# Performance work log

Hardware: AMD Instinct MI355X
Metric: run time of the kernel (lower is better)

Reference implementation:

```python
import jax, jax.numpy as jnp
import numpy as np

N_NODES = 100000
N_EDGES = 1600000
D = 128
EPS = 0.0  # train_eps=False -> constant


def setup_inputs() -> dict:
    key = jax.random.key(0)
    k = jax.random.split(key, 6)
    s = 1.0 / np.sqrt(D)
    return {
        "X": jax.random.normal(k[0], (N_NODES, D), dtype=jnp.float32),
        "W1": jax.random.normal(k[1], (D, D), dtype=jnp.float32) * s,
        "b1": jnp.zeros((D,), dtype=jnp.float32),
        "W2": jax.random.normal(k[2], (D, D), dtype=jnp.float32) * s,
        "b2": jnp.zeros((D,), dtype=jnp.float32),
        "edge_src": jax.random.randint(k[3], (N_EDGES,), 0, N_NODES, dtype=jnp.int32),
        "edge_dst": jax.random.randint(k[4], (N_EDGES,), 0, N_NODES, dtype=jnp.int32),
    }


def reference(X, W1, b1, W2, b2, edge_src, edge_dst):
    # v2v sum aggregation: agg[i] = sum_{j in N(i)} X[j]
    msgs = X[edge_src]  # (E, D) gather
    agg = jax.ops.segment_sum(msgs, edge_dst, num_segments=N_NODES)  # (N, D)
    h = (1.0 + EPS) * X + agg
    # MLP: Linear -> ReLU -> Linear
    h = jax.nn.relu(h @ W1 + b1)
    out = h @ W2 + b2
    return out
```

## Files before the change

### kernel.cpp

```cpp
#include <hip/hip_runtime.h>
#include <hip/hip_bf16.h>

#define N_NODES 100000
#define N_EDGES 1600000
#define D 128

#define NBINS 196
#define BINSHIFT 9
#define EPB 8192
#define RBLK 196
#define EBUF_CAP 8960

#define MID_SORT_BLOCKS 196
#define MID_W_BLOCKS 8
#define MID_CVT_BLOCKS 3125

#define PADK 136

typedef __bf16 bf16x8 __attribute__((ext_vector_type(8)));
typedef short short8 __attribute__((ext_vector_type(8)));
typedef float f32x4 __attribute__((ext_vector_type(4)));

__device__ __forceinline__ unsigned short f2bf(float f) {
  union { float f; unsigned u; } c; c.f = f;
  unsigned u = c.u;
  u += 0x7FFFu + ((u >> 16) & 1u);
  return (unsigned short)(u >> 16);
}
__device__ __forceinline__ float bflo(unsigned u) {
  union { unsigned u; float f; } c; c.u = u << 16; return c.f;
}
__device__ __forceinline__ float bfhi(unsigned u) {
  union { unsigned u; float f; } c; c.u = u & 0xFFFF0000u; return c.f;
}

__launch_bounds__(512)
__global__ void k_bin2(const int* __restrict__ esrc, const int* __restrict__ edst,
                       unsigned* __restrict__ binbuf, int* __restrict__ cntmatT,
                       int* __restrict__ startmatT) {
  __shared__ unsigned lbuf[EPB];
  __shared__ int cnt[NBINS];
  __shared__ int base[NBINS];
  __shared__ int cur[NBINS];
  __shared__ int scanb[256];
  const int b = blockIdx.x, t = threadIdx.x;
  const int e0 = b * EPB;
  const int ne = min(EPB, N_EDGES - e0);

  for (int i = t; i < NBINS; i += 512) { cnt[i] = 0; cur[i] = 0; }
  __syncthreads();
  for (int i = t; i < ne; i += 512)
    atomicAdd(&cnt[edst[e0 + i] >> BINSHIFT], 1);
  __syncthreads();
  if (t < 256) scanb[t] = (t < NBINS) ? cnt[t] : 0;
  __syncthreads();
  for (int d = 1; d < 256; d <<= 1) {
    int x = 0;
    if (t < 256 && t >= d) x = scanb[t - d];
    __syncthreads();
    if (t < 256) scanb[t] += x;
    __syncthreads();
  }
  if (t < NBINS) base[t] = scanb[t] - cnt[t];
  __syncthreads();
  for (int i = t; i < ne; i += 512) {
    int d = edst[e0 + i];
    int s = esrc[e0 + i];
    int bi = d >> BINSHIFT;
    int pos = base[bi] + atomicAdd(&cur[bi], 1);
    lbuf[pos] = ((unsigned)(d & 511) << 17) | (unsigned)s;
  }
  __syncthreads();
  uint4* dst4 = (uint4*)(binbuf + (size_t)b * EPB);
  const uint4* src4 = (const uint4*)lbuf;
  for (int i = t; i < EPB / 4; i += 512) dst4[i] = src4[i];
  if (t < NBINS) {
    cntmatT[t * RBLK + b] = cnt[t];
    startmatT[t * RBLK + b] = base[t];
  }
}

__launch_bounds__(512)
__global__ void k_mid(const unsigned* __restrict__ binbuf, const int* __restrict__ cntmatT,
                      const int* __restrict__ startmatT,
                      int* __restrict__ srt, int* __restrict__ deg, int* __restrict__ offs,
                      const float* __restrict__ X, unsigned short* __restrict__ Xb,
                      const float* __restrict__ W1, const float* __restrict__ W2,
                      unsigned short* __restrict__ Wimg) {
  const int b = blockIdx.x, t = threadIdx.x;

  if (b < MID_SORT_BLOCKS) {
    __shared__ unsigned ebuf[EBUF_CAP];
    __shared__ int hist[512];
    __shared__ int scn[512];
    __shared__ int rcnt[RBLK];
    __shared__ int roff[RBLK];
    __shared__ int eoff[RBLK];
    __shared__ int colsc[256];

    for (int r = t; r < RBLK; r += 512) {
      rcnt[r] = cntmatT[b * RBLK + r];
      roff[r] = startmatT[b * RBLK + r];
    }
    int cs = 0;
    if (t < NBINS) {
      const uint4* row = (const uint4*)(cntmatT + t * RBLK);
#pragma unroll 7
      for (int j = 0; j < RBLK / 4; ++j) {
        uint4 v = row[j];
        cs += (int)(v.x + v.y + v.z + v.w);
      }
    }
    if (t < 256) colsc[t] = (t < NBINS) ? cs : 0;
    __syncthreads();
    for (int d = 1; d < 256; d <<= 1) {
      int x = 0;
      if (t < 256 && t >= d) x = colsc[t - d];
      __syncthreads();
      if (t < 256) colsc[t] += x;
      __syncthreads();
    }
    const int total = cntmatT ? 0 : 0;
    (void)total;
    const int mytotal_holder = 0; (void)mytotal_holder;
    __syncthreads();
    const int mytotal = colsc[b] - ((b == 0) ? 0 : colsc[b - 1]);
    const int gbase = (b == 0) ? 0 : colsc[b - 1];

    if (t < 256) scn[t] = (t < RBLK) ? rcnt[t] : 0;
    __syncthreads();
    for (int d = 1; d < 256; d <<= 1) {
      int x = 0;
      if (t < 256 && t >= d) x = scn[t - d];
      __syncthreads();
      if (t < 256) scn[t] += x;
      __syncthreads();
    }
    if (t < RBLK) eoff[t] = scn[t] - rcnt[t];
    __syncthreads();

    const int wv = t >> 6, ln = t & 63;
    for (int r = wv; r < RBLK; r += 8) {
      const unsigned* src = binbuf + (size_t)r * EPB + roff[r];
      int c = rcnt[r], o = eoff[r];
      for (int i = ln; i < c; i += 64) ebuf[o + i] = src[i];
    }
    hist[t] = 0;
    __syncthreads();

    for (int i = t; i < mytotal; i += 512)
      atomicAdd(&hist[ebuf[i] >> 17], 1);
    __syncthreads();
    int v = hist[t];
    scn[t] = v;
    __syncthreads();
    for (int d = 1; d < 512; d <<= 1) {
      int x = (t >= d) ? scn[t - d] : 0;
      __syncthreads();
      scn[t] += x;
      __syncthreads();
    }
    int n = (b << BINSHIFT) + t;
    if (n < N_NODES) {
      deg[n] = v;
      offs[n] = gbase + scn[t] - v;
    }
    hist[t] = scn[t] - v;
    __syncthreads();
    for (int i = t; i < mytotal; i += 512) {
      unsigned e = ebuf[i];
      int pos = atomicAdd(&hist[e >> 17], 1);
      srt[gbase + pos] = (int)(e & 0x1FFFFu);
    }
    return;
  }
  if (b < MID_SORT_BLOCKS + MID_W_BLOCKS) {
    int bb = b - MID_SORT_BLOCKS;
    const float* W = (bb & 4) ? W2 : W1;
    unsigned short* img = Wimg + ((bb & 4) ? 128 * PADK : 0);
    int k0 = (bb & 3) * 32;
#pragma unroll
    for (int it = 0; it < 8; ++it) {
      int idx = it * 512 + t;
      int k = k0 + (idx >> 7), n = idx & 127;
      img[n * PADK + k] = f2bf(W[k * 128 + n]);
    }
    return;
  }
  size_t i = ((size_t)(b - MID_SORT_BLOCKS - MID_W_BLOCKS) * 512 + t) * 8;
  const float4* p = (const float4*)(X + i);
  float4 a = p[0], c = p[1];
  short8 s;
  s[0] = f2bf(a.x); s[1] = f2bf(a.y); s[2] = f2bf(a.z); s[3] = f2bf(a.w);
  s[4] = f2bf(c.x); s[5] = f2bf(c.y); s[6] = f2bf(c.z); s[7] = f2bf(c.w);
  *(short8*)(Xb + i) = s;
}

__global__ void k_gather_bf(const unsigned int* __restrict__ X1,
                            const int* __restrict__ deg, const int* __restrict__ offs,
                            const int* __restrict__ srt, unsigned int* __restrict__ h0) {
  int node = blockIdx.x * 4 + (threadIdx.x >> 6);
  int lane = threadIdx.x & 63;
  unsigned u = X1[(size_t)node * 64 + lane];
  float hx = bflo(u), hy = bfhi(u);
  int e = offs[node];
  int end = e + deg[node];
  for (; e + 8 <= end; e += 8) {
    int s0 = srt[e],     s1 = srt[e + 1], s2 = srt[e + 2], s3 = srt[e + 3];
    int s4 = srt[e + 4], s5 = srt[e + 5], s6 = srt[e + 6], s7 = srt[e + 7];
    unsigned u0 = X1[(size_t)s0 * 64 + lane];
    unsigned u1 = X1[(size_t)s1 * 64 + lane];
    unsigned u2 = X1[(size_t)s2 * 64 + lane];
    unsigned u3 = X1[(size_t)s3 * 64 + lane];
    unsigned u4 = X1[(size_t)s4 * 64 + lane];
    unsigned u5 = X1[(size_t)s5 * 64 + lane];
    unsigned u6 = X1[(size_t)s6 * 64 + lane];
    unsigned u7 = X1[(size_t)s7 * 64 + lane];
    hx += bflo(u0); hy += bfhi(u0);
    hx += bflo(u1); hy += bfhi(u1);
    hx += bflo(u2); hy += bfhi(u2);
    hx += bflo(u3); hy += bfhi(u3);
    hx += bflo(u4); hy += bfhi(u4);
    hx += bflo(u5); hy += bfhi(u5);
    hx += bflo(u6); hy += bfhi(u6);
    hx += bflo(u7); hy += bfhi(u7);
  }
  for (; e + 2 <= end; e += 2) {
    unsigned u0 = X1[(size_t)srt[e] * 64 + lane];
    unsigned u1 = X1[(size_t)srt[e + 1] * 64 + lane];
    hx += bflo(u0); hy += bfhi(u0);
    hx += bflo(u1); hy += bfhi(u1);
  }
  for (; e < end; ++e) {
    unsigned u0 = X1[(size_t)srt[e] * 64 + lane];
    hx += bflo(u0); hy += bfhi(u0);
  }
  h0[(size_t)node * 64 + lane] = ((unsigned)f2bf(hy) << 16) | f2bf(hx);
}

#define BR2 128

__launch_bounds__(512, 4)
__global__ void k_mlp2(const unsigned short* __restrict__ h0,
                       const unsigned short* __restrict__ Wimg,
                       const float* __restrict__ b1v, const float* __restrict__ b2v,
                       float* __restrict__ out) {
  __shared__ __attribute__((aligned(16))) unsigned short lW[128 * PADK];
  __shared__ __attribute__((aligned(16))) unsigned short lH[BR2 * PADK];

  const int t = threadIdx.x;
  const int wave = t >> 6, lane = t & 63;
  const int lr = lane & 15, lg = lane >> 4;
  const int row0 = blockIdx.x * BR2;
  const int wrow = row0 + wave * 16;

  const uint4* wi = (const uint4*)Wimg;
  uint4* lw = (uint4*)lW;

  for (int i = t; i < 2176; i += 512) lw[i] = wi[i];

  bf16x8 a[4];
#pragma unroll
  for (int kb = 0; kb < 4; ++kb) {
    int r = wrow + lr;
    if (r >= N_NODES) r = N_NODES - 1;
    a[kb] = __builtin_bit_cast(bf16x8,
        *(const short8*)(h0 + (size_t)r * D + kb * 32 + lg * 8));
  }

  f32x4 acc[8];
#pragma unroll
  for (int nc = 0; nc < 8; ++nc) {
    float bb = b1v[nc * 16 + lr];
    acc[nc] = (f32x4){bb, bb, bb, bb};
  }

  __syncthreads();

#pragma unroll
  for (int nc = 0; nc < 8; ++nc) {
#pragma unroll
    for (int kb = 0; kb < 4; ++kb) {
      bf16x8 b = *(const bf16x8*)&lW[(nc * 16 + lr) * PADK + kb * 32 + lg * 8];
      acc[nc] = __builtin_amdgcn_mfma_f32_16x16x32_bf16(a[kb], b, acc[nc], 0, 0, 0);
    }
  }

  __syncthreads();

  {
    const uint4* wi2 = (const uint4*)Wimg + 2176;
    for (int i = t; i < 2176; i += 512) lw[i] = wi2[i];
  }

#pragma unroll
  for (int nc = 0; nc < 8; ++nc) {
#pragma unroll
    for (int r = 0; r < 4; ++r) {
      float v = acc[nc][r];
      v = v > 0.f ? v : 0.f;
      lH[(wave * 16 + lg * 4 + r) * PADK + nc * 16 + lr] = f2bf(v);
    }
  }

  __syncthreads();

  bf16x8 a2[4];
#pragma unroll
  for (int kb = 0; kb < 4; ++kb)
    a2[kb] = *(const bf16x8*)&lH[(wave * 16 + lr) * PADK + kb * 32 + lg * 8];

#pragma unroll
  for (int nc = 0; nc < 8; ++nc) {
    float bb = b2v[nc * 16 + lr];
    acc[nc] = (f32x4){bb, bb, bb, bb};
  }

#pragma unroll
  for (int nc = 0; nc < 8; ++nc) {
#pragma unroll
    for (int kb = 0; kb < 4; ++kb) {
      bf16x8 b = *(const bf16x8*)&lW[(nc * 16 + lr) * PADK + kb * 32 + lg * 8];
      acc[nc] = __builtin_amdgcn_mfma_f32_16x16x32_bf16(a2[kb], b, acc[nc], 0, 0, 0);
    }
  }

#pragma unroll
  for (int nc = 0; nc < 8; ++nc) {
#pragma unroll
    for (int r = 0; r < 4; ++r) {
      int row = wrow + lg * 4 + r;
      if (row < N_NODES) out[(size_t)row * D + nc * 16 + lr] = acc[nc][r];
    }
  }
}


__global__ void k_hist(const int* __restrict__ dst, int* __restrict__ deg) {
  int i = blockIdx.x * 256 + threadIdx.x;
  if (i < N_EDGES) atomicAdd(&deg[dst[i]], 1);
}

__global__ void k_scan1(const int* __restrict__ deg, int* __restrict__ offs,
                        int* __restrict__ bsum) {
  __shared__ int s[1024];
  int t = threadIdx.x;
  int i = blockIdx.x * 1024 + t;
  int v = (i < N_NODES) ? deg[i] : 0;
  s[t] = v;
  __syncthreads();
  for (int d = 1; d < 1024; d <<= 1) {
    int x = (t >= d) ? s[t - d] : 0;
    __syncthreads();
    s[t] += x;
    __syncthreads();
  }
  if (i < N_NODES) offs[i] = s[t] - v;
  if (t == 1023) bsum[blockIdx.x] = s[t];
}

__global__ void k_scan2(int* __restrict__ bsum) {
  __shared__ int s[128];
  int t = threadIdx.x;
  int v = (t < 98) ? bsum[t] : 0;
  s[t] = v;
  __syncthreads();
  for (int d = 1; d < 128; d <<= 1) {
    int x = (t >= d) ? s[t - d] : 0;
    __syncthreads();
    s[t] += x;
    __syncthreads();
  }
  if (t < 98) bsum[t] = s[t] - v;
}

__global__ void k_scan3(int* __restrict__ offs, const int* __restrict__ bsum) {
  int i = blockIdx.x * 1024 + threadIdx.x;
  if (i < N_NODES) offs[i] += bsum[blockIdx.x];
}

__global__ void k_bucket(const int* __restrict__ src, const int* __restrict__ dst,
                         int* __restrict__ offs, int* __restrict__ srt) {
  int i = blockIdx.x * 256 + threadIdx.x;
  if (i < N_EDGES) {
    int pos = atomicAdd(&offs[dst[i]], 1);
    srt[pos] = src[i];
  }
}

__global__ void k_gather(const float* __restrict__ X, const int* __restrict__ deg,
                         const int* __restrict__ offs, const int* __restrict__ srt,
                         float* __restrict__ out) {
  int node = blockIdx.x * 4 + (threadIdx.x >> 6);
  int lane = threadIdx.x & 63;
  const float2* X2 = (const float2*)X;
  float2 h = X2[(size_t)node * 64 + lane];
  int end = offs[node];
  int dg = deg[node];
  for (int e = end - dg; e < end; ++e) {
    int s = srt[e];
    float2 x = X2[(size_t)s * 64 + lane];
    h.x += x.x; h.y += x.y;
  }
  ((float2*)out)[(size_t)node * 64 + lane] = h;
}

#define BR 256

__launch_bounds__(512, 1)
__global__ void k_mlp(const float* __restrict__ h0,
                      const float* __restrict__ W1, const float* __restrict__ b1,
                      const float* __restrict__ W2, const float* __restrict__ b2,
                      float* __restrict__ out) {
  __shared__ __attribute__((aligned(16))) unsigned short lW[2 * 128 * PADK];
  __shared__ __attribute__((aligned(16))) unsigned short lH[BR * PADK];

  const int t = threadIdx.x;
  const int wave = t >> 6, lane = t & 63;
  const int lr = lane & 15, lg = lane >> 4;
  const int row0 = blockIdx.x * BR;
  const int wrow = row0 + wave * 32;

  for (int i = t; i < 128 * 128; i += 512) {
    int k = i >> 7, n = i & 127;
    lW[n * PADK + k] = f2bf(W1[i]);
    lW[128 * PADK + n * PADK + k] = f2bf(W2[i]);
  }

  bf16x8 a[2][4];
#pragma unroll
  for (int tr = 0; tr < 2; ++tr) {
#pragma unroll
    for (int kb = 0; kb < 4; ++kb) {
      int r = wrow + tr * 16 + lr;
      if (r >= N_NODES) r = N_NODES - 1;
      const float4* p = (const float4*)(h0 + (size_t)r * D + kb * 32 + lg * 8);
      float4 f0 = p[0], f1 = p[1];
      short8 s;
      s[0] = f2bf(f0.x); s[1] = f2bf(f0.y); s[2] = f2bf(f0.z); s[3] = f2bf(f0.w);
      s[4] = f2bf(f1.x); s[5] = f2bf(f1.y); s[6] = f2bf(f1.z); s[7] = f2bf(f1.w);
      a[tr][kb] = __builtin_bit_cast(bf16x8, s);
    }
  }

  f32x4 acc[2][8];
#pragma unroll
  for (int nc = 0; nc < 8; ++nc) {
    float bb = b1[nc * 16 + lr];
#pragma unroll
    for (int tr = 0; tr < 2; ++tr) acc[tr][nc] = (f32x4){bb, bb, bb, bb};
  }

  __syncthreads();

#pragma unroll
  for (int nc = 0; nc < 8; ++nc) {
#pragma unroll
    for (int kb = 0; kb < 4; ++kb) {
      bf16x8 b = *(const bf16x8*)&lW[(nc * 16 + lr) * PADK + kb * 32 + lg * 8];
#pragma unroll
      for (int tr = 0; tr < 2; ++tr)
        acc[tr][nc] = __builtin_amdgcn_mfma_f32_16x16x32_bf16(a[tr][kb], b, acc[tr][nc], 0, 0, 0);
    }
  }

#pragma unroll
  for (int tr = 0; tr < 2; ++tr) {
#pragma unroll
    for (int nc = 0; nc < 8; ++nc) {
#pragma unroll
      for (int r = 0; r < 4; ++r) {
        float v = acc[tr][nc][r];
        v = v > 0.f ? v : 0.f;
        int lrow = wave * 32 + tr * 16 + lg * 4 + r;
        lH[lrow * PADK + nc * 16 + lr] = f2bf(v);
      }
    }
  }

  __syncthreads();

  bf16x8 a2[2][4];
#pragma unroll
  for (int tr = 0; tr < 2; ++tr) {
#pragma unroll
    for (int kb = 0; kb < 4; ++kb)
      a2[tr][kb] = *(const bf16x8*)&lH[(wave * 32 + tr * 16 + lr) * PADK + kb * 32 + lg * 8];
  }

#pragma unroll
  for (int nc = 0; nc < 8; ++nc) {
    float bb = b2[nc * 16 + lr];
#pragma unroll
    for (int tr = 0; tr < 2; ++tr) acc[tr][nc] = (f32x4){bb, bb, bb, bb};
  }

#pragma unroll
  for (int nc = 0; nc < 8; ++nc) {
#pragma unroll
    for (int kb = 0; kb < 4; ++kb) {
      bf16x8 b = *(const bf16x8*)&lW[128 * PADK + (nc * 16 + lr) * PADK + kb * 32 + lg * 8];
#pragma unroll
      for (int tr = 0; tr < 2; ++tr)
        acc[tr][nc] = __builtin_amdgcn_mfma_f32_16x16x32_bf16(a2[tr][kb], b, acc[tr][nc], 0, 0, 0);
    }
  }

#pragma unroll
  for (int tr = 0; tr < 2; ++tr) {
#pragma unroll
    for (int nc = 0; nc < 8; ++nc) {
#pragma unroll
      for (int r = 0; r < 4; ++r) {
        int row = wrow + tr * 16 + lg * 4 + r;
        if (row < N_NODES) out[(size_t)row * D + nc * 16 + lr] = acc[tr][nc][r];
      }
    }
  }
}

extern "C" void kernel_launch(void* const* d_in, const int* in_sizes, int n_in,
                              void* d_out, int out_size, void* d_ws, size_t ws_size,
                              hipStream_t stream) {
  const float* X  = (const float*)d_in[0];
  const float* W1 = (const float*)d_in[1];
  const float* b1 = (const float*)d_in[2];
  const float* W2 = (const float*)d_in[3];
  const float* b2 = (const float*)d_in[4];
  const int* esrc = (const int*)d_in[5];
  const int* edst = (const int*)d_in[6];
  float* out = (float*)d_out;

  char* ws = (char*)d_ws;
  int* deg      = (int*)(ws);
  int* offs     = (int*)(ws + 400000);
  int* srt      = (int*)(ws + 800000);
  unsigned short* Xb  = (unsigned short*)(ws + 7200000);
  unsigned short* h0b = (unsigned short*)(ws + 32800000);
  unsigned* binbuf = (unsigned*)(ws + 32800000);
  int* cntmatT   = (int*)(ws + 32800000 + 6422528);
  int* startmatT = (int*)(ws + 32800000 + 6422528 + 153664);
  unsigned short* Wimg = (unsigned short*)(ws + 58400000);
  const size_t NEED = 58469632;

  if (ws_size >= NEED) {
    k_bin2<<<RBLK, 512, 0, stream>>>(esrc, edst, binbuf, cntmatT, startmatT);
    k_mid<<<MID_SORT_BLOCKS + MID_W_BLOCKS + MID_CVT_BLOCKS, 512, 0, stream>>>(
        binbuf, cntmatT, startmatT, srt, deg, offs, X, Xb, W1, W2, Wimg);
    k_gather_bf<<<N_NODES / 4, 256, 0, stream>>>((const unsigned*)Xb, deg, offs, srt,
                                                 (unsigned*)h0b);
    k_mlp2<<<(N_NODES + BR2 - 1) / BR2, 512, 0, stream>>>(h0b, Wimg, b1, b2, out);
  } else {
    int* bsum  = (int*)(ws + 800000);
    int* srtF  = (int*)(ws + 802048);
    hipMemsetAsync(deg, 0, N_NODES * sizeof(int), stream);
    k_hist  <<<N_EDGES / 256, 256, 0, stream>>>(edst, deg);
    k_scan1 <<<98, 1024, 0, stream>>>(deg, offs, bsum);
    k_scan2 <<<1, 128, 0, stream>>>(bsum);
    k_scan3 <<<98, 1024, 0, stream>>>(offs, bsum);
    k_bucket<<<N_EDGES / 256, 256, 0, stream>>>(esrc, edst, offs, srtF);
    k_gather<<<N_NODES / 4, 256, 0, stream>>>(X, deg, offs, srtF, out);
    k_mlp   <<<(N_NODES + BR - 1) / BR, 512, 0, stream>>>(out, W1, b1, W2, b2, out);
  }
}
```

Before: 132.3 us.

## Fuse per-bin edge sort with neighbor gather and merge binning with conversions

The edge binning pass is merged with the X and W bf16 conversion into one head kernel. The per-bin counting sort and the neighbor gather are fused into a single 1024-thread block per bin, so sorted source indices stay in shared memory instead of round-tripping through global srt/deg/offs arrays. This removes one launch and the global sorted-index traffic. In exchange the latency-bound gather now runs on only 196 blocks, each wave walking 32 nodes in sequence, which cuts parallelism and occupancy compared with the previous 25k-block gather.

```diff
diff --git a/kernel.cpp b/kernel.cpp
--- a/kernel.cpp
+++ b/kernel.cpp
@@ -11,9 +11,8 @@
 #define RBLK 196
 #define EBUF_CAP 8960
 
-#define MID_SORT_BLOCKS 196
-#define MID_W_BLOCKS 8
-#define MID_CVT_BLOCKS 3125
+#define HEAD_W_BLOCKS 8
+#define HEAD_CVT_BLOCKS 3125
 
 #define PADK 136
 
@@ -35,147 +34,58 @@
 }
 
 __launch_bounds__(512)
-__global__ void k_bin2(const int* __restrict__ esrc, const int* __restrict__ edst,
+__global__ void k_head(const int* __restrict__ esrc, const int* __restrict__ edst,
                        unsigned* __restrict__ binbuf, int* __restrict__ cntmatT,
-                       int* __restrict__ startmatT) {
-  __shared__ unsigned lbuf[EPB];
-  __shared__ int cnt[NBINS];
-  __shared__ int base[NBINS];
-  __shared__ int cur[NBINS];
-  __shared__ int scanb[256];
+                       int* __restrict__ startmatT,
+                       const float* __restrict__ X, unsigned short* __restrict__ Xb,
+                       const float* __restrict__ W1, const float* __restrict__ W2,
+                       unsigned short* __restrict__ Wimg) {
   const int b = blockIdx.x, t = threadIdx.x;
-  const int e0 = b * EPB;
-  const int ne = min(EPB, N_EDGES - e0);
-
-  for (int i = t; i < NBINS; i += 512) { cnt[i] = 0; cur[i] = 0; }
-  __syncthreads();
-  for (int i = t; i < ne; i += 512)
-    atomicAdd(&cnt[edst[e0 + i] >> BINSHIFT], 1);
-  __syncthreads();
-  if (t < 256) scanb[t] = (t < NBINS) ? cnt[t] : 0;
-  __syncthreads();
-  for (int d = 1; d < 256; d <<= 1) {
-    int x = 0;
-    if (t < 256 && t >= d) x = scanb[t - d];
-    __syncthreads();
-    if (t < 256) scanb[t] += x;
-    __syncthreads();
-  }
-  if (t < NBINS) base[t] = scanb[t] - cnt[t];
-  __syncthreads();
-  for (int i = t; i < ne; i += 512) {
-    int d = edst[e0 + i];
-    int s = esrc[e0 + i];
-    int bi = d >> BINSHIFT;
-    int pos = base[bi] + atomicAdd(&cur[bi], 1);
-    lbuf[pos] = ((unsigned)(d & 511) << 17) | (unsigned)s;
-  }
-  __syncthreads();
-  uint4* dst4 = (uint4*)(binbuf + (size_t)b * EPB);
-  const uint4* src4 = (const uint4*)lbuf;
-  for (int i = t; i < EPB / 4; i += 512) dst4[i] = src4[i];
-  if (t < NBINS) {
-    cntmatT[t * RBLK + b] = cnt[t];
-    startmatT[t * RBLK + b] = base[t];
-  }
-}
-
-__launch_bounds__(512)
-__global__ void k_mid(const unsigned* __restrict__ binbuf, const int* __restrict__ cntmatT,
-                      const int* __restrict__ startmatT,
-                      int* __restrict__ srt, int* __restrict__ deg, int* __restrict__ offs,
-                      const float* __restrict__ X, unsigned short* __restrict__ Xb,
-                      const float* __restrict__ W1, const float* __restrict__ W2,
-                      unsigned short* __restrict__ Wimg) {
-  const int b = blockIdx.x, t = threadIdx.x;
-
-  if (b < MID_SORT_BLOCKS) {
-    __shared__ unsigned ebuf[EBUF_CAP];
-    __shared__ int hist[512];
-    __shared__ int scn[512];
-    __shared__ int rcnt[RBLK];
-    __shared__ int roff[RBLK];
-    __shared__ int eoff[RBLK];
-    __shared__ int colsc[256];
-
-    for (int r = t; r < RBLK; r += 512) {
-      rcnt[r] = cntmatT[b * RBLK + r];
-      roff[r] = startmatT[b * RBLK + r];
-    }
-    int cs = 0;
-    if (t < NBINS) {
-      const uint4* row = (const uint4*)(cntmatT + t * RBLK);
-#pragma unroll 7
-      for (int j = 0; j < RBLK / 4; ++j) {
-        uint4 v = row[j];
-        cs += (int)(v.x + v.y + v.z + v.w);
-      }
-    }
-    if (t < 256) colsc[t] = (t < NBINS) ? cs : 0;
+
+  if (b < RBLK) {
+    __shared__ unsigned lbuf[EPB];
+    __shared__ int cnt[NBINS];
+    __shared__ int base[NBINS];
+    __shared__ int cur[NBINS];
+    __shared__ int scanb[256];
+    const int e0 = b * EPB;
+    const int ne = min(EPB, N_EDGES - e0);
+
+    for (int i = t; i < NBINS; i += 512) { cnt[i] = 0; cur[i] = 0; }
+    __syncthreads();
+    for (int i = t; i < ne; i += 512)
+      atomicAdd(&cnt[edst[e0 + i] >> BINSHIFT], 1);
+    __syncthreads();
+    if (t < 256) scanb[t] = (t < NBINS) ? cnt[t] : 0;
     __syncthreads();
     for (int d = 1; d < 256; d <<= 1) {
       int x = 0;
-      if (t < 256 && t >= d) x = colsc[t - d];
+      if (t < 256 && t >= d) x = scanb[t - d];
       __syncthreads();
-      if (t < 256) colsc[t] += x;
+      if (t < 256) scanb[t] += x;
       __syncthreads();
     }
-    const int total = cntmatT ? 0 : 0;
-    (void)total;
-    const int mytotal_holder = 0; (void)mytotal_holder;
-    __syncthreads();
-    const int mytotal = colsc[b] - ((b == 0) ? 0 : colsc[b - 1]);
-    const int gbase = (b == 0) ? 0 : colsc[b - 1];
-
-    if (t < 256) scn[t] = (t < RBLK) ? rcnt[t] : 0;
-    __syncthreads();
-    for (int d = 1; d < 256; d <<= 1) {
-      int x = 0;
-      if (t < 256 && t >= d) x = scn[t - d];
-      __syncthreads();
-      if (t < 256) scn[t] += x;
-      __syncthreads();
-    }
-    if (t < RBLK) eoff[t] = scn[t] - rcnt[t];
-    __syncthreads();
-
-    const int wv = t >> 6, ln = t & 63;
-    for (int r = wv; r < RBLK; r += 8) {
-      const unsigned* src = binbuf + (size_t)r * EPB + roff[r];
-      int c = rcnt[r], o = eoff[r];
-      for (int i = ln; i < c; i += 64) ebuf[o + i] = src[i];
-    }
-    hist[t] = 0;
-    __syncthreads();
-
-    for (int i = t; i < mytotal; i += 512)
-      atomicAdd(&hist[ebuf[i] >> 17], 1);
-    __syncthreads();
-    int v = hist[t];
-    scn[t] = v;
-    __syncthreads();
-    for (int d = 1; d < 512; d <<= 1) {
-      int x = (t >= d) ? scn[t - d] : 0;
-      __syncthreads();
-      scn[t] += x;
-      __syncthreads();
-    }
-    int n = (b << BINSHIFT) + t;
-    if (n < N_NODES) {
-      deg[n] = v;
-      offs[n] = gbase + scn[t] - v;
-    }
-    hist[t] = scn[t] - v;
-    __syncthreads();
-    for (int i = t; i < mytotal; i += 512) {
-      unsigned e = ebuf[i];
-      int pos = atomicAdd(&hist[e >> 17], 1);
-      srt[gbase + pos] = (int)(e & 0x1FFFFu);
+    if (t < NBINS) base[t] = scanb[t] - cnt[t];
+    __syncthreads();
+    for (int i = t; i < ne; i += 512) {
+      int d = edst[e0 + i];
+      int s = esrc[e0 + i];
+      int bi = d >> BINSHIFT;
+      int pos = base[bi] + atomicAdd(&cur[bi], 1);
+      lbuf[pos] = ((unsigned)(d & 511) << 17) | (unsigned)s;
+    }
+    __syncthreads();
+    uint4* dst4 = (uint4*)(binbuf + (size_t)b * EPB);
+    const uint4* src4 = (const uint4*)lbuf;
+    for (int i = t; i < EPB / 4; i += 512) dst4[i] = src4[i];
+    if (t < NBINS) {
+      cntmatT[t * RBLK + b] = cnt[t];
+      startmatT[t * RBLK + b] = base[t];
     }
     return;
   }
-  if (b < MID_SORT_BLOCKS + MID_W_BLOCKS) {
-    int bb = b - MID_SORT_BLOCKS;
+  if (b < RBLK + HEAD_W_BLOCKS) {
+    int bb = b - RBLK;
     const float* W = (bb & 4) ? W2 : W1;
     unsigned short* img = Wimg + ((bb & 4) ? 128 * PADK : 0);
     int k0 = (bb & 3) * 32;
@@ -187,7 +97,7 @@
     }
     return;
   }
-  size_t i = ((size_t)(b - MID_SORT_BLOCKS - MID_W_BLOCKS) * 512 + t) * 8;
+  size_t i = ((size_t)(b - RBLK - HEAD_W_BLOCKS) * 512 + t) * 8;
   const float4* p = (const float4*)(X + i);
   float4 a = p[0], c = p[1];
   short8 s;
@@ -196,46 +106,121 @@
   *(short8*)(Xb + i) = s;
 }
 
-__global__ void k_gather_bf(const unsigned int* __restrict__ X1,
-                            const int* __restrict__ deg, const int* __restrict__ offs,
-                            const int* __restrict__ srt, unsigned int* __restrict__ h0) {
-  int node = blockIdx.x * 4 + (threadIdx.x >> 6);
-  int lane = threadIdx.x & 63;
-  unsigned u = X1[(size_t)node * 64 + lane];
-  float hx = bflo(u), hy = bfhi(u);
-  int e = offs[node];
-  int end = e + deg[node];
-  for (; e + 8 <= end; e += 8) {
-    int s0 = srt[e],     s1 = srt[e + 1], s2 = srt[e + 2], s3 = srt[e + 3];
-    int s4 = srt[e + 4], s5 = srt[e + 5], s6 = srt[e + 6], s7 = srt[e + 7];
-    unsigned u0 = X1[(size_t)s0 * 64 + lane];
-    unsigned u1 = X1[(size_t)s1 * 64 + lane];
-    unsigned u2 = X1[(size_t)s2 * 64 + lane];
-    unsigned u3 = X1[(size_t)s3 * 64 + lane];
-    unsigned u4 = X1[(size_t)s4 * 64 + lane];
-    unsigned u5 = X1[(size_t)s5 * 64 + lane];
-    unsigned u6 = X1[(size_t)s6 * 64 + lane];
-    unsigned u7 = X1[(size_t)s7 * 64 + lane];
-    hx += bflo(u0); hy += bfhi(u0);
-    hx += bflo(u1); hy += bfhi(u1);
-    hx += bflo(u2); hy += bfhi(u2);
-    hx += bflo(u3); hy += bfhi(u3);
-    hx += bflo(u4); hy += bfhi(u4);
-    hx += bflo(u5); hy += bfhi(u5);
-    hx += bflo(u6); hy += bfhi(u6);
-    hx += bflo(u7); hy += bfhi(u7);
-  }
-  for (; e + 2 <= end; e += 2) {
-    unsigned u0 = X1[(size_t)srt[e] * 64 + lane];
-    unsigned u1 = X1[(size_t)srt[e + 1] * 64 + lane];
-    hx += bflo(u0); hy += bfhi(u0);
-    hx += bflo(u1); hy += bfhi(u1);
-  }
-  for (; e < end; ++e) {
-    unsigned u0 = X1[(size_t)srt[e] * 64 + lane];
-    hx += bflo(u0); hy += bfhi(u0);
-  }
-  h0[(size_t)node * 64 + lane] = ((unsigned)f2bf(hy) << 16) | f2bf(hx);
+__launch_bounds__(1024)
+__global__ void k_sortgather(const unsigned* __restrict__ binbuf,
+                             const int* __restrict__ cntmatT,
+                             const int* __restrict__ startmatT,
+                             const unsigned* __restrict__ X1,
+                             unsigned* __restrict__ h0) {
+  __shared__ unsigned ebuf[EBUF_CAP];
+  __shared__ unsigned ebuf2[EBUF_CAP];
+  __shared__ int hist[512];
+  __shared__ int scn[512];
+  __shared__ int nstart[512];
+  __shared__ int ncnt[512];
+  __shared__ int rcnt[RBLK];
+  __shared__ int roff[RBLK];
+  __shared__ int eoff[RBLK];
+  __shared__ int s_total;
+
+  const int b = blockIdx.x, t = threadIdx.x;
+  const int n0 = b << BINSHIFT;
+  const int wv = t >> 6, ln = t & 63;
+
+  for (int r = t; r < RBLK; r += 1024) {
+    rcnt[r] = cntmatT[b * RBLK + r];
+    roff[r] = startmatT[b * RBLK + r];
+  }
+  __syncthreads();
+
+  if (t < 256) scn[t] = (t < RBLK) ? rcnt[t] : 0;
+  __syncthreads();
+  for (int d = 1; d < 256; d <<= 1) {
+    int x = 0;
+    if (t < 256 && t >= d) x = scn[t - d];
+    __syncthreads();
+    if (t < 256) scn[t] += x;
+    __syncthreads();
+  }
+  if (t < RBLK) eoff[t] = scn[t] - rcnt[t];
+  if (t == RBLK - 1) s_total = scn[t];
+  __syncthreads();
+  const int mytotal = s_total;
+
+  for (int r = wv; r < RBLK; r += 16) {
+    const unsigned* src = binbuf + (size_t)r * EPB + roff[r];
+    int c = rcnt[r], o = eoff[r];
+    for (int i = ln; i < c; i += 64) ebuf[o + i] = src[i];
+  }
+  if (t < 512) hist[t] = 0;
+  __syncthreads();
+
+  for (int i = t; i < mytotal; i += 1024)
+    atomicAdd(&hist[ebuf[i] >> 17], 1);
+  __syncthreads();
+  int v = (t < 512) ? hist[t] : 0;
+  if (t < 512) scn[t] = v;
+  __syncthreads();
+  for (int d = 1; d < 512; d <<= 1) {
+    int x = 0;
+    if (t < 512 && t >= d) x = scn[t - d];
+    __syncthreads();
+    if (t < 512) scn[t] += x;
+    __syncthreads();
+  }
+  if (t < 512) {
+    nstart[t] = scn[t] - v;
+    ncnt[t] = v;
+    hist[t] = scn[t] - v;
+  }
+  __syncthreads();
+  for (int i = t; i < mytotal; i += 1024) {
+    unsigned e = ebuf[i];
+    int pos = atomicAdd(&hist[e >> 17], 1);
+    ebuf2[pos] = e & 0x1FFFFu;
+  }
+  __syncthreads();
+
+  for (int j = 0; j < 32; ++j) {
+    int li = wv * 32 + j;
+    int node = n0 + li;
+    if (node >= N_NODES) break;
+    unsigned u = X1[(size_t)node * 64 + ln];
+    float hx = bflo(u), hy = bfhi(u);
+    int e = nstart[li];
+    int end = e + ncnt[li];
+    for (; e + 8 <= end; e += 8) {
+      int s0 = ebuf2[e],     s1 = ebuf2[e + 1], s2 = ebuf2[e + 2], s3 = ebuf2[e + 3];
+      int s4 = ebuf2[e + 4], s5 = ebuf2[e + 5], s6 = ebuf2[e + 6], s7 = ebuf2[e + 7];
+      unsigned u0 = X1[(size_t)s0 * 64 + ln];
+      unsigned u1 = X1[(size_t)s1 * 64 + ln];
+      unsigned u2 = X1[(size_t)s2 * 64 + ln];
+      unsigned u3 = X1[(size_t)s3 * 64 + ln];
+      unsigned u4 = X1[(size_t)s4 * 64 + ln];
+      unsigned u5 = X1[(size_t)s5 * 64 + ln];
+      unsigned u6 = X1[(size_t)s6 * 64 + ln];
+      unsigned u7 = X1[(size_t)s7 * 64 + ln];
+      hx += bflo(u0); hy += bfhi(u0);
+      hx += bflo(u1); hy += bfhi(u1);
+      hx += bflo(u2); hy += bfhi(u2);
+      hx += bflo(u3); hy += bfhi(u3);
+      hx += bflo(u4); hy += bfhi(u4);
+      hx += bflo(u5); hy += bfhi(u5);
+      hx += bflo(u6); hy += bfhi(u6);
+      hx += bflo(u7); hy += bfhi(u7);
+    }
+    for (; e + 2 <= end; e += 2) {
+      unsigned u0 = X1[(size_t)ebuf2[e] * 64 + ln];
+      unsigned u1 = X1[(size_t)ebuf2[e + 1] * 64 + ln];
+      hx += bflo(u0); hy += bfhi(u0);
+      hx += bflo(u1); hy += bfhi(u1);
+    }
+    for (; e < end; ++e) {
+      unsigned u0 = X1[(size_t)ebuf2[e] * 64 + ln];
+      hx += bflo(u0); hy += bfhi(u0);
+    }
+    h0[(size_t)node * 64 + ln] = ((unsigned)f2bf(hy) << 16) | f2bf(hx);
+  }
 }
 
 #define BR2 128
@@ -532,27 +517,25 @@
   float* out = (float*)d_out;
 
   char* ws = (char*)d_ws;
-  int* deg      = (int*)(ws);
-  int* offs     = (int*)(ws + 400000);
-  int* srt      = (int*)(ws + 800000);
-  unsigned short* Xb  = (unsigned short*)(ws + 7200000);
-  unsigned short* h0b = (unsigned short*)(ws + 32800000);
-  unsigned* binbuf = (unsigned*)(ws + 32800000);
-  int* cntmatT   = (int*)(ws + 32800000 + 6422528);
-  int* startmatT = (int*)(ws + 32800000 + 6422528 + 153664);
-  unsigned short* Wimg = (unsigned short*)(ws + 58400000);
-  const size_t NEED = 58469632;
+  unsigned* binbuf = (unsigned*)(ws);
+  int* cntmatT   = (int*)(ws + 6422528);
+  int* startmatT = (int*)(ws + 6576192);
+  unsigned short* Xb  = (unsigned short*)(ws + 6729856);
+  unsigned short* h0b = (unsigned short*)(ws + 32329856);
+  unsigned short* Wimg = (unsigned short*)(ws + 57929856);
+  const size_t NEED = 57999488;
 
   if (ws_size >= NEED) {
-    k_bin2<<<RBLK, 512, 0, stream>>>(esrc, edst, binbuf, cntmatT, startmatT);
-    k_mid<<<MID_SORT_BLOCKS + MID_W_BLOCKS + MID_CVT_BLOCKS, 512, 0, stream>>>(
-        binbuf, cntmatT, startmatT, srt, deg, offs, X, Xb, W1, W2, Wimg);
-    k_gather_bf<<<N_NODES / 4, 256, 0, stream>>>((const unsigned*)Xb, deg, offs, srt,
-                                                 (unsigned*)h0b);
+    k_head<<<RBLK + HEAD_W_BLOCKS + HEAD_CVT_BLOCKS, 512, 0, stream>>>(
+        esrc, edst, binbuf, cntmatT, startmatT, X, Xb, W1, W2, Wimg);
+    k_sortgather<<<NBINS, 1024, 0, stream>>>(binbuf, cntmatT, startmatT,
+                                             (const unsigned*)Xb, (unsigned*)h0b);
     k_mlp2<<<(N_NODES + BR2 - 1) / BR2, 512, 0, stream>>>(h0b, Wimg, b1, b2, out);
   } else {
-    int* bsum  = (int*)(ws + 800000);
-    int* srtF  = (int*)(ws + 802048);
+    int* deg  = (int*)(ws);
+    int* offs = (int*)(ws + 400000);
+    int* bsum = (int*)(ws + 800000);
+    int* srtF = (int*)(ws + 802048);
     hipMemsetAsync(deg, 0, N_NODES * sizeof(int), stream);
     k_hist  <<<N_EDGES / 256, 256, 0, stream>>>(edst, deg);
     k_scan1 <<<98, 1024, 0, stream>>>(deg, offs, bsum);
```

New measurement: 130.2 us, median of 2. Within noise of the previous version (-1.6%).

## Slice bf16 feature matrix into 8 column slices for cache-local gather

Applied to the files above, without the earlier changes.

Stores the bf16 copy of X and the aggregated h0 as eight column slices of 16 features each (32 bytes per node per slice). The gather kernel assigns each block one slice, so the working set per slice (about 3.2 MB) is more likely to stay in cache during the random neighbour reads. Each node is handled by 8 lanes instead of 64. The MLP loader is adapted to read A fragments from the sliced layout. The trade-off is that each edge index is re-read once per slice, and each gather access is a 32-byte segment.

```diff
diff --git a/kernel.cpp b/kernel.cpp
--- a/kernel.cpp
+++ b/kernel.cpp
@@ -13,7 +13,10 @@
 
 #define MID_SORT_BLOCKS 196
 #define MID_W_BLOCKS 8
-#define MID_CVT_BLOCKS 3125
+#define MID_CVT_BLOCKS 1563
+
+#define SLICE_U 800000
+#define SLICE_S 1600000
 
 #define PADK 136
 
@@ -120,10 +123,6 @@
       if (t < 256) colsc[t] += x;
       __syncthreads();
     }
-    const int total = cntmatT ? 0 : 0;
-    (void)total;
-    const int mytotal_holder = 0; (void)mytotal_holder;
-    __syncthreads();
     const int mytotal = colsc[b] - ((b == 0) ? 0 : colsc[b - 1]);
     const int gbase = (b == 0) ? 0 : colsc[b - 1];
 
@@ -187,55 +186,57 @@
     }
     return;
   }
-  size_t i = ((size_t)(b - MID_SORT_BLOCKS - MID_W_BLOCKS) * 512 + t) * 8;
-  const float4* p = (const float4*)(X + i);
-  float4 a = p[0], c = p[1];
-  short8 s;
-  s[0] = f2bf(a.x); s[1] = f2bf(a.y); s[2] = f2bf(a.z); s[3] = f2bf(a.w);
-  s[4] = f2bf(c.x); s[5] = f2bf(c.y); s[6] = f2bf(c.z); s[7] = f2bf(c.w);
-  *(short8*)(Xb + i) = s;
-}
-
-__global__ void k_gather_bf(const unsigned int* __restrict__ X1,
+  int idx = (b - MID_SORT_BLOCKS - MID_W_BLOCKS) * 512 + t;
+  if (idx >= N_NODES * 8) return;
+  int n = idx >> 3, sl = idx & 7;
+  const float4* p = (const float4*)(X + (size_t)n * D + sl * 16);
+  float4 a0 = p[0], a1 = p[1], a2 = p[2], a3 = p[3];
+  short8 s0, s1;
+  s0[0] = f2bf(a0.x); s0[1] = f2bf(a0.y); s0[2] = f2bf(a0.z); s0[3] = f2bf(a0.w);
+  s0[4] = f2bf(a1.x); s0[5] = f2bf(a1.y); s0[6] = f2bf(a1.z); s0[7] = f2bf(a1.w);
+  s1[0] = f2bf(a2.x); s1[1] = f2bf(a2.y); s1[2] = f2bf(a2.z); s1[3] = f2bf(a2.w);
+  s1[4] = f2bf(a3.x); s1[5] = f2bf(a3.y); s1[6] = f2bf(a3.z); s1[7] = f2bf(a3.w);
+  unsigned short* dst = Xb + (size_t)sl * SLICE_S + (size_t)n * 16;
+  *(short8*)dst = s0;
+  *(short8*)(dst + 8) = s1;
+}
+
+__launch_bounds__(512)
+__global__ void k_gather_sl(const unsigned* __restrict__ Xs,
                             const int* __restrict__ deg, const int* __restrict__ offs,
-                            const int* __restrict__ srt, unsigned int* __restrict__ h0) {
-  int node = blockIdx.x * 4 + (threadIdx.x >> 6);
-  int lane = threadIdx.x & 63;
-  unsigned u = X1[(size_t)node * 64 + lane];
-  float hx = bflo(u), hy = bfhi(u);
-  int e = offs[node];
-  int end = e + deg[node];
-  for (; e + 8 <= end; e += 8) {
-    int s0 = srt[e],     s1 = srt[e + 1], s2 = srt[e + 2], s3 = srt[e + 3];
-    int s4 = srt[e + 4], s5 = srt[e + 5], s6 = srt[e + 6], s7 = srt[e + 7];
-    unsigned u0 = X1[(size_t)s0 * 64 + lane];
-    unsigned u1 = X1[(size_t)s1 * 64 + lane];
-    unsigned u2 = X1[(size_t)s2 * 64 + lane];
-    unsigned u3 = X1[(size_t)s3 * 64 + lane];
-    unsigned u4 = X1[(size_t)s4 * 64 + lane];
-    unsigned u5 = X1[(size_t)s5 * 64 + lane];
-    unsigned u6 = X1[(size_t)s6 * 64 + lane];
-    unsigned u7 = X1[(size_t)s7 * 64 + lane];
-    hx += bflo(u0); hy += bfhi(u0);
-    hx += bflo(u1); hy += bfhi(u1);
-    hx += bflo(u2); hy += bfhi(u2);
-    hx += bflo(u3); hy += bfhi(u3);
-    hx += bflo(u4); hy += bfhi(u4);
-    hx += bflo(u5); hy += bfhi(u5);
-    hx += bflo(u6); hy += bfhi(u6);
-    hx += bflo(u7); hy += bfhi(u7);
-  }
-  for (; e + 2 <= end; e += 2) {
-    unsigned u0 = X1[(size_t)srt[e] * 64 + lane];
-    unsigned u1 = X1[(size_t)srt[e + 1] * 64 + lane];
-    hx += bflo(u0); hy += bfhi(u0);
-    hx += bflo(u1); hy += bfhi(u1);
-  }
-  for (; e < end; ++e) {
-    unsigned u0 = X1[(size_t)srt[e] * 64 + lane];
-    hx += bflo(u0); hy += bfhi(u0);
-  }
-  h0[(size_t)node * 64 + lane] = ((unsigned)f2bf(hy) << 16) | f2bf(hx);
+                            const int* __restrict__ srt, unsigned* __restrict__ h0s) {
+  const int sl = blockIdx.x & 7;
+  const int chunk = blockIdx.x >> 3;
+  const int t = threadIdx.x;
+  const int G = t >> 3, l8 = t & 7;
+  const unsigned* Xsl = Xs + (size_t)sl * SLICE_U;
+  unsigned* h0sl = h0s + (size_t)sl * SLICE_U;
+
+#pragma unroll
+  for (int j = 0; j < 4; ++j) {
+    int node = chunk * 256 + j * 64 + G;
+    if (node >= N_NODES) break;
+    unsigned u = Xsl[node * 8 + l8];
+    float hx = bflo(u), hy = bfhi(u);
+    int e = offs[node];
+    int end = e + deg[node];
+    for (; e + 4 <= end; e += 4) {
+      int s0 = srt[e], s1 = srt[e + 1], s2 = srt[e + 2], s3 = srt[e + 3];
+      unsigned u0 = Xsl[s0 * 8 + l8];
+      unsigned u1 = Xsl[s1 * 8 + l8];
+      unsigned u2 = Xsl[s2 * 8 + l8];
+      unsigned u3 = Xsl[s3 * 8 + l8];
+      hx += bflo(u0); hy += bfhi(u0);
+      hx += bflo(u1); hy += bfhi(u1);
+      hx += bflo(u2); hy += bfhi(u2);
+      hx += bflo(u3); hy += bfhi(u3);
+    }
+    for (; e < end; ++e) {
+      unsigned u0 = Xsl[srt[e] * 8 + l8];
+      hx += bflo(u0); hy += bfhi(u0);
+    }
+    h0sl[node * 8 + l8] = ((unsigned)f2bf(hy) << 16) | f2bf(hx);
+  }
 }
 
 #define BR2 128
@@ -264,8 +265,9 @@
   for (int kb = 0; kb < 4; ++kb) {
     int r = wrow + lr;
     if (r >= N_NODES) r = N_NODES - 1;
+    int slc = kb * 2 + (lg >> 1);
     a[kb] = __builtin_bit_cast(bf16x8,
-        *(const short8*)(h0 + (size_t)r * D + kb * 32 + lg * 8));
+        *(const short8*)(h0 + (size_t)slc * SLICE_S + (size_t)r * 16 + (lg & 1) * 8));
   }
 
   f32x4 acc[8];
@@ -547,12 +549,12 @@
     k_bin2<<<RBLK, 512, 0, stream>>>(esrc, edst, binbuf, cntmatT, startmatT);
     k_mid<<<MID_SORT_BLOCKS + MID_W_BLOCKS + MID_CVT_BLOCKS, 512, 0, stream>>>(
         binbuf, cntmatT, startmatT, srt, deg, offs, X, Xb, W1, W2, Wimg);
-    k_gather_bf<<<N_NODES / 4, 256, 0, stream>>>((const unsigned*)Xb, deg, offs, srt,
-                                                 (unsigned*)h0b);
+    k_gather_sl<<<((N_NODES + 255) / 256) * 8, 512, 0, stream>>>(
+        (const unsigned*)Xb, deg, offs, srt, (unsigned*)h0b);
     k_mlp2<<<(N_NODES + BR2 - 1) / BR2, 512, 0, stream>>>(h0b, Wimg, b1, b2, out);
   } else {
-    int* bsum  = (int*)(ws + 800000);
-    int* srtF  = (int*)(ws + 802048);
+    int* bsum = (int*)(ws + 800000);
+    int* srtF = (int*)(ws + 802048);
     hipMemsetAsync(deg, 0, N_NODES * sizeof(int), stream);
     k_hist  <<<N_EDGES / 256, 256, 0, stream>>>(edst, deg);
     k_scan1 <<<98, 1024, 0, stream>>>(deg, offs, bsum);
```

Result: slower. 170.0 us (+28.5%).
